# Kernel tuning notes

Hardware: AMD Instinct MI355X
Metric: run time of the kernel (lower is better)

The kernel has to match this reference:

```python
import jax, jax.numpy as jnp
import numpy as np

MARGIN = 0.4
SCALE = 80.0
NEG_FILL = -1e30  # used instead of -inf for masked logsumexp (keeps grads NaN-free)

N, D, NUM_CLASSES = 8192, 128, 512


def setup_inputs() -> dict:
    key = jax.random.key(0)
    k1, k2 = jax.random.split(key)
    embeds = jax.random.normal(k1, (N, D), dtype=jnp.float32)
    labels = jax.random.randint(k2, (N,), 0, NUM_CLASSES, dtype=jnp.int64)
    return {"embeds": embeds, "labels": labels}


def _masked_lse(terms, mask):
    # stable logsumexp over axis=1 restricted to mask
    t = jnp.where(mask, terms, NEG_FILL)
    m = jnp.max(t, axis=1, keepdims=True)
    return jnp.squeeze(m, 1) + jnp.log(jnp.sum(jnp.exp(t - m), axis=1))


def reference(embeds, labels):
    # L2-normalize embeddings (F.normalize, p=2, dim=1, eps=1e-12)
    norm = jnp.maximum(jnp.linalg.norm(embeds, axis=1, keepdims=True), 1e-12)
    e = embeds / norm
    sim = e @ e.T  # [N, N]

    same = labels[:, None] == labels[None, :]
    eye = jnp.eye(labels.shape[0], dtype=bool)
    pos_mask = same & ~eye          # positives for each anchor (row)
    neg_mask = ~same                # negatives for each anchor

    # alphas are computed under no_grad in the original
    ap_alpha = jax.lax.stop_gradient(jax.nn.relu(1.0 + MARGIN - sim))
    an_alpha = jax.lax.stop_gradient(jax.nn.relu(sim + MARGIN))

    ap_term = -SCALE * ap_alpha * (sim - 1.0 + MARGIN)
    an_term = SCALE * an_alpha * (sim - MARGIN)

    np_cnt = jnp.sum(pos_mask, axis=1)  # positives per anchor
    nn_cnt = jnp.sum(neg_mask, axis=1)  # negatives per anchor
    valid = (np_cnt > 0) & (nn_cnt > 0)

    # All-triplets logsumexp factorizes: LSE over (p,n) pairs of ap_term[p]
    # equals LSE over p + log(num_neg); symmetric for an_term.
    lse_p = _masked_lse(ap_term, pos_mask)
    lse_n = _masked_lse(an_term, neg_mask)
    log_np = jnp.where(valid, jnp.log(np_cnt.astype(sim.dtype)), 0.0)
    log_nn = jnp.where(valid, jnp.log(nn_cnt.astype(sim.dtype)), 0.0)

    loss_i = jax.nn.softplus(lse_p + log_nn + lse_n + log_np)
    loss = jnp.sum(jnp.where(valid, loss_i, 0.0)) / jnp.maximum(
        jnp.sum(valid).astype(sim.dtype), 1.0)
    return loss
```

## Files before the change

### kernel.cpp

```cpp
#include <hip/hip_runtime.h>
#include <hip/hip_bf16.h>

#define NN_ 8192
#define DD_ 128
#define NCLS 512
#define NSPLIT 32
#define JSPLIT (NN_ / NSPLIT)

typedef short bf16x8 __attribute__((ext_vector_type(8)));
typedef float f32x4 __attribute__((ext_vector_type(4)));

union U4 { uint4 u; bf16x8 h; };

#if __has_builtin(__builtin_amdgcn_exp2f)
#define EXP2(x) __builtin_amdgcn_exp2f(x)
#else
#define EXP2(x) __expf((x) * 0.69314718056f)
#endif

#define C1 115.415603f
#define C2 96.9491065f
#define LN2 0.69314718056f

__device__ __forceinline__ unsigned short f2bf(float f) {
    unsigned int u = __float_as_uint(f);
    unsigned int r = (u + 0x7FFFu + ((u >> 16) & 1u)) >> 16;
    return (unsigned short)r;
}


__global__ __launch_bounds__(1024) void k_sorthead(const int* __restrict__ labels,
                                                   int* __restrict__ start,
                                                   int* __restrict__ base) {
    __shared__ int hist[NCLS];
    __shared__ int wsum[8];
    int t = threadIdx.x;
    if (t < NCLS) hist[t] = 0;
    __syncthreads();
    int4 la = ((const int4*)labels)[t * 2];
    int4 lb = ((const int4*)labels)[t * 2 + 1];
    atomicAdd(&hist[la.x], 1);
    atomicAdd(&hist[la.y], 1);
    atomicAdd(&hist[la.z], 1);
    atomicAdd(&hist[la.w], 1);
    atomicAdd(&hist[lb.x], 1);
    atomicAdd(&hist[lb.y], 1);
    atomicAdd(&hist[lb.z], 1);
    atomicAdd(&hist[lb.w], 1);
    __syncthreads();
    int v = (t < NCLS) ? hist[t] : 0;
    int x = v;
#pragma unroll
    for (int m = 1; m < 64; m <<= 1) {
        int y = __shfl_up(x, m);
        if ((t & 63) >= m) x += y;
    }
    if (t < NCLS && (t & 63) == 63) wsum[t >> 6] = x;
    __syncthreads();
    if (t < NCLS) {
        int w = t >> 6, woff = 0;
#pragma unroll
        for (int k = 0; k < 8; k++)
            if (k < w) woff += wsum[k];
        int excl = woff + x - v;
        start[t] = excl;
        base[t] = excl;
        if (t == 0) start[NCLS] = NN_;
    }
}

__global__ __launch_bounds__(256) void k_scatter(const int* __restrict__ labels,
                                                 int* __restrict__ base,
                                                 int* __restrict__ srcrow,
                                                 int* __restrict__ plab) {
    int row = blockIdx.x * 256 + threadIdx.x;
    int l = labels[row];
    int p = atomicAdd(&base[l], 1);
    srcrow[p] = row;
    plab[p] = l;
}

__global__ __launch_bounds__(256) void k_norm(const float* __restrict__ x,
                                              const int* __restrict__ srcrow,
                                              unsigned short* __restrict__ ebf) {
    int t = threadIdx.x;
    int r16 = t >> 4;
    int g = t & 15;
    int slot = blockIdx.x * 16 + r16;
    int orig = srcrow[slot];
    const float4* xr = (const float4*)(x + (size_t)orig * DD_);
    float4 v0 = xr[g * 2];
    float4 v1 = xr[g * 2 + 1];
    float ss = v0.x * v0.x + v0.y * v0.y + v0.z * v0.z + v0.w * v0.w +
               v1.x * v1.x + v1.y * v1.y + v1.z * v1.z + v1.w * v1.w;
#pragma unroll
    for (int m = 1; m < 16; m <<= 1) ss += __shfl_xor(ss, m);
    float inv = 1.0f / fmaxf(sqrtf(ss), 1e-12f);
    float vs[8] = {v0.x, v0.y, v0.z, v0.w, v1.x, v1.y, v1.z, v1.w};
    unsigned int p[4];
#pragma unroll
    for (int k = 0; k < 4; k++) {
        unsigned short lo = f2bf(vs[2 * k] * inv);
        unsigned short hi = f2bf(vs[2 * k + 1] * inv);
        p[k] = (unsigned int)lo | ((unsigned int)hi << 16);
    }
    uint4 out = {p[0], p[1], p[2], p[3]};
    ((uint4*)ebf)[blockIdx.x * 256 + g * 16 + r16] = out;
}

__global__ __launch_bounds__(512, 4) void k_main(const unsigned short* __restrict__ ebf,
                                                 const int* __restrict__ plab,
                                                 const int* __restrict__ start,
                                                 float* __restrict__ states) {
    __shared__ uint4 bsh[2048];

    const int tid = threadIdx.x;
    const int lane = tid & 63;
    const int wave = tid >> 6;
    const int quad = lane >> 4;
    const int lcol = lane & 15;
    const int rowbase = blockIdx.y * 256 + wave * 32;
    const int jsplit = blockIdx.x;
    const int j0 = jsplit * JSPLIT;

    const uint4* fb = (const uint4*)ebf;

    U4 afr[2][4];
#pragma unroll
    for (int g = 0; g < 2; g++)
#pragma unroll
        for (int kc = 0; kc < 4; kc++)
            afr[g][kc].u = fb[((rowbase >> 4) + g) * 256 + kc * 64 + lane];

    int il[2][4];
#pragma unroll
    for (int g = 0; g < 2; g++)
#pragma unroll
        for (int r = 0; r < 4; r++) il[g][r] = plab[rowbase + g * 16 + quad * 4 + r];

    int labmin = __builtin_amdgcn_readfirstlane(plab[rowbase]);
    int labmax = __builtin_amdgcn_readfirstlane(plab[rowbase + 31]);
    int lo = __builtin_amdgcn_readfirstlane(start[labmin]);
    int hi = __builtin_amdgcn_readfirstlane(start[labmax + 1]);

    float S_an[2][4], m_p[2][4], s_p[2][4];
#pragma unroll
    for (int g = 0; g < 2; g++)
#pragma unroll
        for (int r = 0; r < 4; r++) {
            S_an[g][r] = 0.f;
            m_p[g][r] = -1e30f;
            s_p[g][r] = 0.f;
        }

    const f32x4 Z = {0.f, 0.f, 0.f, 0.f};

    {
        const int tb = (j0 >> 4) * 256;
        bsh[tid] = fb[tb + tid];
        bsh[tid + 512] = fb[tb + tid + 512];
    }
    __syncthreads();

    const int NIT = JSPLIT / 64;
    for (int it = 0; it < NIT; ++it) {
        const int cur = it & 1;
        const int jt = j0 + it * 64;
        const bool has = (it + 1 < NIT);

        uint4 stg0, stg1;
        if (has) {
            const int tn = ((jt + 64) >> 4) * 256;
            stg0 = fb[tn + tid];
            stg1 = fb[tn + tid + 512];
        }

        const int bbase = (cur << 10) + lane;

#pragma unroll
        for (int c = 0; c < 4; c++) {
            U4 bf[4];
#pragma unroll
            for (int kc = 0; kc < 4; kc++) bf[kc].u = bsh[bbase + c * 256 + kc * 64];
            f32x4 acc0 = __builtin_amdgcn_mfma_f32_16x16x32_bf16(afr[0][0].h, bf[0].h, Z, 0, 0, 0);
            f32x4 acc1 = __builtin_amdgcn_mfma_f32_16x16x32_bf16(afr[1][0].h, bf[0].h, Z, 0, 0, 0);
#pragma unroll
            for (int kc = 1; kc < 4; kc++) {
                acc0 = __builtin_amdgcn_mfma_f32_16x16x32_bf16(afr[0][kc].h, bf[kc].h, acc0, 0, 0, 0);
                acc1 = __builtin_amdgcn_mfma_f32_16x16x32_bf16(afr[1][kc].h, bf[kc].h, acc1, 0, 0, 0);
            }
            const int jc = jt + c * 16;
            if (jc < hi && jc + 16 > lo) {
                int jl = plab[jc + lcol];
                int j = jc + lcol;
#pragma unroll
                for (int g = 0; g < 2; g++) {
#pragma unroll
                    for (int r = 0; r < 4; r++) {
                        float s = (g == 0) ? acc0[r] : acc1[r];
                        int i = rowbase + g * 16 + quad * 4 + r;
                        bool same = (jl == il[g][r]);
                        float u = fmaxf(s, -0.4f);
                        float e = EXP2(fmaf(u * C1, u, -C1));
                        S_an[g][r] += same ? 0.0f : e;
                        if (same && j != i) {
                            float al = fmaxf(1.4f - s, 0.0f) * (-C1);
                            float tp = al * (s - 0.6f);
                            float mn = fmaxf(m_p[g][r], tp);
                            s_p[g][r] = s_p[g][r] * EXP2(m_p[g][r] - mn) + EXP2(tp - mn);
                            m_p[g][r] = mn;
                        }
                    }
                }
            } else {
#pragma unroll
                for (int r = 0; r < 4; r++) {
                    float u0 = fmaxf(acc0[r], -0.4f);
                    S_an[0][r] += EXP2(fmaf(u0 * C1, u0, -C1));
                    float u1 = fmaxf(acc1[r], -0.4f);
                    S_an[1][r] += EXP2(fmaf(u1 * C1, u1, -C1));
                }
            }
        }

        if (has) {
            bsh[((cur ^ 1) << 10) + tid] = stg0;
            bsh[((cur ^ 1) << 10) + tid + 512] = stg1;
        }
        __syncthreads();
    }

#pragma unroll
    for (int g = 0; g < 2; g++)
#pragma unroll
        for (int r = 0; r < 4; r++) {
#pragma unroll
            for (int m = 1; m < 16; m <<= 1) {
                S_an[g][r] += __shfl_xor(S_an[g][r], m);
                float m2 = __shfl_xor(m_p[g][r], m);
                float s2 = __shfl_xor(s_p[g][r], m);
                float mn = fmaxf(m_p[g][r], m2);
                s_p[g][r] = s_p[g][r] * EXP2(m_p[g][r] - mn) + s2 * EXP2(m2 - mn);
                m_p[g][r] = mn;
            }
        }
    if (lcol == 0) {
#pragma unroll
        for (int g = 0; g < 2; g++)
#pragma unroll
            for (int r = 0; r < 4; r++) {
                int i = rowbase + g * 16 + quad * 4 + r;
                float4 st = {m_p[g][r], s_p[g][r], S_an[g][r], 0.f};
                ((float4*)states)[(size_t)i * NSPLIT + jsplit] = st;
            }
    }
}

__global__ __launch_bounds__(256) void k_fin(const float* __restrict__ states,
                                             const int* __restrict__ plab,
                                             const int* __restrict__ start,
                                             float* __restrict__ partials) {
    int i = blockIdx.x * 256 + threadIdx.x;
    float m_p = -1e30f, s_p = 0.f, S_an = 0.f;
#pragma unroll
    for (int k = 0; k < NSPLIT; k++) {
        float4 st = ((const float4*)states)[(size_t)i * NSPLIT + k];
        S_an += st.z;
        float mn = fmaxf(m_p, st.x);
        s_p = s_p * EXP2(m_p - mn) + st.y * EXP2(st.x - mn);
        m_p = mn;
    }
    int l = plab[i];
    int sz = start[l + 1] - start[l];
    int np = sz - 1;
    int nn = NN_ - sz;
    float loss = 0.0f, v = 0.0f;
    if (np > 0 && nn > 0 && s_p > 0.f && S_an > 0.f) {
        float lse_p = LN2 * m_p + __logf(s_p);
        float lse_n = 67.2f + __logf(S_an);
        float z = lse_p + lse_n + __logf((float)np) + __logf((float)nn);
        loss = fmaxf(z, 0.0f) + log1pf(__expf(-fabsf(z)));
        v = 1.0f;
    }
#pragma unroll
    for (int m = 1; m < 64; m <<= 1) {
        loss += __shfl_xor(loss, m);
        v += __shfl_xor(v, m);
    }
    if ((threadIdx.x & 63) == 0) {
        int w = (blockIdx.x << 2) | (threadIdx.x >> 6);
        partials[w * 2] = loss;
        partials[w * 2 + 1] = v;
    }
}

__global__ void k_div(const float* __restrict__ partials, float* __restrict__ out) {
    int t = threadIdx.x;
    float loss = partials[t * 2] + partials[(t + 64) * 2];
    float v = partials[t * 2 + 1] + partials[(t + 64) * 2 + 1];
#pragma unroll
    for (int m = 1; m < 64; m <<= 1) {
        loss += __shfl_xor(loss, m);
        v += __shfl_xor(v, m);
    }
    if (t == 0) out[0] = loss / fmaxf(v, 1.0f);
}

extern "C" void kernel_launch(void* const* d_in, const int* in_sizes, int n_in,
                              void* d_out, int out_size, void* d_ws, size_t ws_size,
                              hipStream_t stream) {
    const float* embeds = (const float*)d_in[0];
    const int* labels = (const int*)d_in[1];
    float* out = (float*)d_out;

    char* ws = (char*)d_ws;
    unsigned short* ebf = (unsigned short*)ws;
    float* states = (float*)(ws + 2097152);
    float* partials = (float*)(ws + 6291456);
    int* srcrow = (int*)(ws + 6292480);
    int* plab = (int*)(ws + 6325248);
    int* start = (int*)(ws + 6358016);
    int* base = (int*)(ws + 6360068);

    k_sorthead<<<1, 1024, 0, stream>>>(labels, start, base);
    k_scatter<<<NN_ / 256, 256, 0, stream>>>(labels, base, srcrow, plab);
    k_norm<<<NN_ / 16, 256, 0, stream>>>(embeds, srcrow, ebf);
    k_main<<<dim3(NSPLIT, NN_ / 256), 512, 0, stream>>>(ebf, plab, start, states);
    k_fin<<<NN_ / 256, 256, 0, stream>>>(states, plab, start, partials);
    k_div<<<1, 64, 0, stream>>>(partials, out);
}
```

Baseline: 109.1 us.

## Exploit similarity symmetry: compute only upper-triangle tiles and emit column partial states

The main kernel now walks only half of the 64x64 grid of 128x128 tiles, using diagonal offsets d in 0..32. Each tile emits row-wise partial LSE states plus column-wise states reduced across quads, so the mirrored block's contribution comes for free and the MFMA and exp work is roughly halved. The scatter and normalize kernels are merged into one, which removes a launch and the srcrow indirection. In exchange there are extra cross-lane shuffles and column-state writes per chunk, and the finalize kernel must now merge 161 partial states per row instead of 32.

Result: slower. 116.5 us (+6.8%).

```diff
diff --git a/kernel.cpp b/kernel.cpp
--- a/kernel.cpp
+++ b/kernel.cpp
@@ -4,8 +4,8 @@
 #define NN_ 8192
 #define DD_ 128
 #define NCLS 512
-#define NSPLIT 32
-#define JSPLIT (NN_ / NSPLIT)
+#define NB 64
+#define BR 128
 
 typedef short bf16x8 __attribute__((ext_vector_type(8)));
 typedef float f32x4 __attribute__((ext_vector_type(4)));
@@ -19,8 +19,8 @@
 #endif
 
 #define C1 115.415603f
-#define C2 96.9491065f
 #define LN2 0.69314718056f
+#define NEGM -1e30f
 
 __device__ __forceinline__ unsigned short f2bf(float f) {
     unsigned int u = __float_as_uint(f);
@@ -39,14 +39,10 @@
     __syncthreads();
     int4 la = ((const int4*)labels)[t * 2];
     int4 lb = ((const int4*)labels)[t * 2 + 1];
-    atomicAdd(&hist[la.x], 1);
-    atomicAdd(&hist[la.y], 1);
-    atomicAdd(&hist[la.z], 1);
-    atomicAdd(&hist[la.w], 1);
-    atomicAdd(&hist[lb.x], 1);
-    atomicAdd(&hist[lb.y], 1);
-    atomicAdd(&hist[lb.z], 1);
-    atomicAdd(&hist[lb.w], 1);
+    atomicAdd(&hist[la.x], 1); atomicAdd(&hist[la.y], 1);
+    atomicAdd(&hist[la.z], 1); atomicAdd(&hist[la.w], 1);
+    atomicAdd(&hist[lb.x], 1); atomicAdd(&hist[lb.y], 1);
+    atomicAdd(&hist[lb.z], 1); atomicAdd(&hist[lb.w], 1);
     __syncthreads();
     int v = (t < NCLS) ? hist[t] : 0;
     int x = v;
@@ -69,26 +65,35 @@
     }
 }
 
-__global__ __launch_bounds__(256) void k_scatter(const int* __restrict__ labels,
-                                                 int* __restrict__ base,
-                                                 int* __restrict__ srcrow,
-                                                 int* __restrict__ plab) {
-    int row = blockIdx.x * 256 + threadIdx.x;
-    int l = labels[row];
-    int p = atomicAdd(&base[l], 1);
-    srcrow[p] = row;
-    plab[p] = l;
-}
-
-__global__ __launch_bounds__(256) void k_norm(const float* __restrict__ x,
-                                              const int* __restrict__ srcrow,
-                                              unsigned short* __restrict__ ebf) {
+__global__ __launch_bounds__(256) void k_scatnorm(const float* __restrict__ x,
+                                                  const int* __restrict__ labels,
+                                                  int* __restrict__ base,
+                                                  int* __restrict__ plab,
+                                                  unsigned short* __restrict__ ebf,
+                                                  float4* __restrict__ rowstates,
+                                                  float4* __restrict__ colstates) {
+    __shared__ int sp[16];
     int t = threadIdx.x;
+    if (t < 16) {
+        int row = blockIdx.x * 16 + t;
+        int l = labels[row];
+        int p = atomicAdd(&base[l], 1);
+        plab[p] = l;
+        sp[t] = p;
+        float4 neu = {NEGM, 0.f, 0.f, 0.f};
+        if (p >= NN_ / 2) {
+            rowstates[32 * NN_ + p] = neu;
+        } else {
+#pragma unroll
+            for (int w = 0; w < 4; w++)
+                colstates[(31 * 4 + w) * NN_ + p] = neu;
+        }
+    }
+    __syncthreads();
     int r16 = t >> 4;
     int g = t & 15;
-    int slot = blockIdx.x * 16 + r16;
-    int orig = srcrow[slot];
-    const float4* xr = (const float4*)(x + (size_t)orig * DD_);
+    int row = blockIdx.x * 16 + r16;
+    const float4* xr = (const float4*)(x + (size_t)row * DD_);
     float4 v0 = xr[g * 2];
     float4 v1 = xr[g * 2 + 1];
     float ss = v0.x * v0.x + v0.y * v0.y + v0.z * v0.z + v0.w * v0.w +
@@ -105,23 +110,29 @@
         p[k] = (unsigned int)lo | ((unsigned int)hi << 16);
     }
     uint4 out = {p[0], p[1], p[2], p[3]};
-    ((uint4*)ebf)[blockIdx.x * 256 + g * 16 + r16] = out;
-}
-
-__global__ __launch_bounds__(512, 4) void k_main(const unsigned short* __restrict__ ebf,
+    int dst = sp[r16];
+    ((uint4*)ebf)[(dst >> 4) * 256 + g * 16 + (dst & 15)] = out;
+}
+
+__global__ __launch_bounds__(256, 4) void k_main(const unsigned short* __restrict__ ebf,
                                                  const int* __restrict__ plab,
                                                  const int* __restrict__ start,
-                                                 float* __restrict__ states) {
-    __shared__ uint4 bsh[2048];
+                                                 float4* __restrict__ rowstates,
+                                                 float4* __restrict__ colstates) {
+    __shared__ uint4 bsh[1024];
 
     const int tid = threadIdx.x;
     const int lane = tid & 63;
     const int wave = tid >> 6;
     const int quad = lane >> 4;
     const int lcol = lane & 15;
-    const int rowbase = blockIdx.y * 256 + wave * 32;
-    const int jsplit = blockIdx.x;
-    const int j0 = jsplit * JSPLIT;
+    int bid = blockIdx.x;
+    int d, I;
+    if (bid < 2048) { d = bid >> 6; I = bid & 63; }
+    else            { d = 32;       I = bid - 2048; }
+    const int J = (I + d) & 63;
+    const int rowbase = I * BR + wave * 32;
+    const int j0 = J * BR;
 
     const uint4* fb = (const uint4*)ebf;
 
@@ -147,38 +158,34 @@
 #pragma unroll
     for (int g = 0; g < 2; g++)
 #pragma unroll
-        for (int r = 0; r < 4; r++) {
-            S_an[g][r] = 0.f;
-            m_p[g][r] = -1e30f;
-            s_p[g][r] = 0.f;
-        }
+        for (int r = 0; r < 4; r++) { S_an[g][r] = 0.f; m_p[g][r] = NEGM; s_p[g][r] = 0.f; }
 
     const f32x4 Z = {0.f, 0.f, 0.f, 0.f};
 
     {
         const int tb = (j0 >> 4) * 256;
         bsh[tid] = fb[tb + tid];
-        bsh[tid + 512] = fb[tb + tid + 512];
-    }
-    __syncthreads();
-
-    const int NIT = JSPLIT / 64;
-    for (int it = 0; it < NIT; ++it) {
+        bsh[tid + 256] = fb[tb + tid + 256];
+    }
+    __syncthreads();
+
+#pragma unroll
+    for (int it = 0; it < 4; ++it) {
         const int cur = it & 1;
-        const int jt = j0 + it * 64;
-        const bool has = (it + 1 < NIT);
+        const int jt = j0 + it * 32;
+        const bool has = (it < 3);
 
         uint4 stg0, stg1;
         if (has) {
-            const int tn = ((jt + 64) >> 4) * 256;
+            const int tn = ((jt + 32) >> 4) * 256;
             stg0 = fb[tn + tid];
-            stg1 = fb[tn + tid + 512];
-        }
-
-        const int bbase = (cur << 10) + lane;
-
-#pragma unroll
-        for (int c = 0; c < 4; c++) {
+            stg1 = fb[tn + tid + 256];
+        }
+
+        const int bbase = (cur << 9) + lane;
+
+#pragma unroll
+        for (int c = 0; c < 2; c++) {
             U4 bf[4];
 #pragma unroll
             for (int kc = 0; kc < 4; kc++) bf[kc].u = bsh[bbase + c * 256 + kc * 64];
@@ -190,6 +197,7 @@
                 acc1 = __builtin_amdgcn_mfma_f32_16x16x32_bf16(afr[1][kc].h, bf[kc].h, acc1, 0, 0, 0);
             }
             const int jc = jt + c * 16;
+            float cm = NEGM, cs = 0.f, cS = 0.f;
             if (jc < hi && jc + 16 > lo) {
                 int jl = plab[jc + lcol];
                 int j = jc + lcol;
@@ -202,13 +210,19 @@
                         bool same = (jl == il[g][r]);
                         float u = fmaxf(s, -0.4f);
                         float e = EXP2(fmaf(u * C1, u, -C1));
-                        S_an[g][r] += same ? 0.0f : e;
-                        if (same && j != i) {
-                            float al = fmaxf(1.4f - s, 0.0f) * (-C1);
-                            float tp = al * (s - 0.6f);
-                            float mn = fmaxf(m_p[g][r], tp);
-                            s_p[g][r] = s_p[g][r] * EXP2(m_p[g][r] - mn) + EXP2(tp - mn);
-                            m_p[g][r] = mn;
+                        float ee = same ? 0.0f : e;
+                        S_an[g][r] += ee;
+                        cS += ee;
+                        if (same) {
+                            float tp = fmaxf(1.4f - s, 0.0f) * (-C1) * (s - 0.6f);
+                            if (j != i) {
+                                float mn = fmaxf(m_p[g][r], tp);
+                                s_p[g][r] = s_p[g][r] * EXP2(m_p[g][r] - mn) + EXP2(tp - mn);
+                                m_p[g][r] = mn;
+                            }
+                            float mn2 = fmaxf(cm, tp);
+                            cs = cs * EXP2(cm - mn2) + EXP2(tp - mn2);
+                            cm = mn2;
                         }
                     }
                 }
@@ -216,16 +230,35 @@
 #pragma unroll
                 for (int r = 0; r < 4; r++) {
                     float u0 = fmaxf(acc0[r], -0.4f);
-                    S_an[0][r] += EXP2(fmaf(u0 * C1, u0, -C1));
+                    float e0 = EXP2(fmaf(u0 * C1, u0, -C1));
+                    S_an[0][r] += e0;
                     float u1 = fmaxf(acc1[r], -0.4f);
-                    S_an[1][r] += EXP2(fmaf(u1 * C1, u1, -C1));
+                    float e1 = EXP2(fmaf(u1 * C1, u1, -C1));
+                    S_an[1][r] += e1;
+                    cS += e0 + e1;
                 }
             }
+            if (d) {
+#pragma unroll
+                for (int mm = 16; mm < 64; mm <<= 1) {
+                    float m2 = __shfl_xor(cm, mm);
+                    float s2 = __shfl_xor(cs, mm);
+                    float S2 = __shfl_xor(cS, mm);
+                    float mn = fmaxf(cm, m2);
+                    cs = cs * EXP2(cm - mn) + s2 * EXP2(m2 - mn);
+                    cm = mn;
+                    cS += S2;
+                }
+                if (lane < 16) {
+                    float4 st = {cm, cs, cS, 0.f};
+                    colstates[((d - 1) * 4 + wave) * NN_ + jc + lcol] = st;
+                }
+            }
         }
 
         if (has) {
-            bsh[((cur ^ 1) << 10) + tid] = stg0;
-            bsh[((cur ^ 1) << 10) + tid + 512] = stg1;
+            bsh[((cur ^ 1) << 9) + tid] = stg0;
+            bsh[((cur ^ 1) << 9) + tid + 256] = stg1;
         }
         __syncthreads();
     }
@@ -251,20 +284,27 @@
             for (int r = 0; r < 4; r++) {
                 int i = rowbase + g * 16 + quad * 4 + r;
                 float4 st = {m_p[g][r], s_p[g][r], S_an[g][r], 0.f};
-                ((float4*)states)[(size_t)i * NSPLIT + jsplit] = st;
-            }
-    }
-}
-
-__global__ __launch_bounds__(256) void k_fin(const float* __restrict__ states,
-                                             const int* __restrict__ plab,
-                                             const int* __restrict__ start,
-                                             float* __restrict__ partials) {
-    int i = blockIdx.x * 256 + threadIdx.x;
-    float m_p = -1e30f, s_p = 0.f, S_an = 0.f;
-#pragma unroll
-    for (int k = 0; k < NSPLIT; k++) {
-        float4 st = ((const float4*)states)[(size_t)i * NSPLIT + k];
+                rowstates[d * NN_ + i] = st;
+            }
+    }
+}
+
+__global__ __launch_bounds__(64) void k_fin(const float4* __restrict__ rowstates,
+                                            const float4* __restrict__ colstates,
+                                            const int* __restrict__ plab,
+                                            const int* __restrict__ start,
+                                            float* __restrict__ partials) {
+    int i = blockIdx.x * 64 + threadIdx.x;
+    float m_p = NEGM, s_p = 0.f, S_an = 0.f;
+    for (int p = 0; p < 33; p++) {
+        float4 st = rowstates[p * NN_ + i];
+        S_an += st.z;
+        float mn = fmaxf(m_p, st.x);
+        s_p = s_p * EXP2(m_p - mn) + st.y * EXP2(st.x - mn);
+        m_p = mn;
+    }
+    for (int p = 0; p < 128; p++) {
+        float4 st = colstates[p * NN_ + i];
         S_an += st.z;
         float mn = fmaxf(m_p, st.x);
         s_p = s_p * EXP2(m_p - mn) + st.y * EXP2(st.x - mn);
@@ -287,10 +327,9 @@
         loss += __shfl_xor(loss, m);
         v += __shfl_xor(v, m);
     }
-    if ((threadIdx.x & 63) == 0) {
-        int w = (blockIdx.x << 2) | (threadIdx.x >> 6);
-        partials[w * 2] = loss;
-        partials[w * 2 + 1] = v;
+    if (threadIdx.x == 0) {
+        partials[blockIdx.x * 2] = loss;
+        partials[blockIdx.x * 2 + 1] = v;
     }
 }
 
@@ -315,17 +354,16 @@
 
     char* ws = (char*)d_ws;
     unsigned short* ebf = (unsigned short*)ws;
-    float* states = (float*)(ws + 2097152);
-    float* partials = (float*)(ws + 6291456);
-    int* srcrow = (int*)(ws + 6292480);
-    int* plab = (int*)(ws + 6325248);
-    int* start = (int*)(ws + 6358016);
-    int* base = (int*)(ws + 6360068);
+    float4* rowstates = (float4*)(ws + 2097152);
+    float4* colstates = (float4*)(ws + 6422528);
+    float* partials = (float*)(ws + 23199744);
+    int* plab = (int*)(ws + 23200768);
+    int* start = (int*)(ws + 23233536);
+    int* base = (int*)(ws + 23235840);
 
     k_sorthead<<<1, 1024, 0, stream>>>(labels, start, base);
-    k_scatter<<<NN_ / 256, 256, 0, stream>>>(labels, base, srcrow, plab);
-    k_norm<<<NN_ / 16, 256, 0, stream>>>(embeds, srcrow, ebf);
-    k_main<<<dim3(NSPLIT, NN_ / 256), 512, 0, stream>>>(ebf, plab, start, states);
-    k_fin<<<NN_ / 256, 256, 0, stream>>>(states, plab, start, partials);
+    k_scatnorm<<<NN_ / 16, 256, 0, stream>>>(embeds, labels, base, plab, ebf, rowstates, colstates);
+    k_main<<<2080, 256, 0, stream>>>(ebf, plab, start, rowstates, colstates);
+    k_fin<<<NN_ / 64, 64, 0, stream>>>(rowstates, colstates, plab, start, partials);
     k_div<<<1, 64, 0, stream>>>(partials, out);
 }
```
